# Kernel tuning notes

Measured on AMD Instinct MI355X. Metric: run time of the kernel, lower is better.

Reference implementation:

```python
import jax, jax.numpy as jnp
import numpy as np

N = 262144
E = N * 32
C_W = 7.0 / np.pi  # Wendland C2 2D normalization


def kernel_gradient(q, dirs, h):
    # torchSPHv2 wendland gradient: -dir * C/h^3 * 20 q (1-q)^3, q = r/h in [0,1]
    mag = (C_W / h ** 3) * 20.0 * q * (1.0 - q) ** 3
    return -dirs * mag[:, None]


def setup_inputs() -> dict:
    key = jax.random.key(0)
    ks = jax.random.split(key, 10)
    pos = lambda k: jax.random.uniform(k, (N,), dtype=jnp.float32) + 0.5  # keep strictly positive
    fluidArea = pos(ks[0]) * 1e-3
    fluidActualArea = pos(ks[1]) * 1e-3
    fluidRestDensity = pos(ks[2]) * 1000.0
    fluidDensity = pos(ks[3])
    fluidPressure2 = jax.random.uniform(ks[4], (N,), dtype=jnp.float32) * 1e3
    fluidPredictedVelocity = jax.random.normal(ks[5], (N, 2), dtype=jnp.float32)
    fluidPredAccel = jax.random.normal(ks[6], (N, 2), dtype=jnp.float32)
    fluidNeighbors = jax.random.randint(ks[7], (2, E), 0, N, dtype=jnp.int32)
    fluidRadialDistances = jax.random.uniform(ks[8], (E,), dtype=jnp.float32)
    d = jax.random.normal(ks[9], (E, 2), dtype=jnp.float32)
    fluidDistances = d / (jnp.linalg.norm(d, axis=1, keepdims=True) + 1e-7)
    return {
        'fluidArea': fluidArea, 'fluidActualArea': fluidActualArea,
        'fluidRestDensity': fluidRestDensity, 'fluidDensity': fluidDensity,
        'fluidPressure2': fluidPressure2,
        'fluidPredictedVelocity': fluidPredictedVelocity,
        'fluidPredAccel': fluidPredAccel,
        'fluidRadialDistances': fluidRadialDistances,
        'fluidDistances': fluidDistances,
        'fluidNeighbors': fluidNeighbors,
        'support': 0.05, 'dt': 0.002,
    }


def reference(fluidArea, fluidActualArea, fluidRestDensity, fluidDensity,
              fluidPressure2, fluidPredictedVelocity, fluidPredAccel,
              fluidRadialDistances, fluidDistances, fluidNeighbors,
              support, dt):
    seg = lambda v, i: jax.ops.segment_sum(v, i, num_segments=N)
    i = fluidNeighbors[0]
    j = fluidNeighbors[1]
    grad = kernel_gradient(fluidRadialDistances, fluidDistances, support)  # [E,2]
    grad2 = jnp.einsum('nd,nd->n', grad, grad)

    # --- alpha (fluid term + final) ---
    kSum1 = seg(fluidActualArea[j][:, None] * grad, i)                       # [N,2]
    kSum2 = seg((fluidActualArea ** 2 / (fluidArea * fluidRestDensity))[j] * grad2, i)
    fac = -dt ** 2 * fluidActualArea
    mass = fluidArea * fluidRestDensity
    alpha = fac / mass * jnp.einsum('nd,nd->n', kSum1, kSum1) + fac * kSum2

    # --- fluid pressure acceleration ---
    facA = -(fluidArea * fluidRestDensity)[j]
    p = fluidPressure2 / (fluidDensity * fluidRestDensity) ** 2
    fluidAccelTerm = seg((facA * (p[i] + p[j]))[:, None] * grad, i)          # [N,2]

    # --- source term (velocity divergence) ---
    facS = -dt * fluidActualArea[j]
    vij = fluidPredictedVelocity[i] - fluidPredictedVelocity[j]
    source = seg(facS * jnp.einsum('nd,nd->n', vij, grad), i)                # [N]

    # --- updated pressure fluid kernel sum ---
    facP = dt ** 2 * fluidActualArea[j]
    aij = fluidPredAccel[i] - fluidPredAccel[j]
    kernelSum = seg(jnp.einsum('nd,nd->n', facP[:, None] * aij, grad), i)    # [N]

    return jnp.concatenate([alpha[:, None], fluidAccelTerm,
                            source[:, None], kernelSum[:, None]], axis=1)  # [N,5]
```

## Files before the change

### kernel.cpp

```cpp
#include <hip/hip_runtime.h>
#include <math.h>


#define PB        512
#define PB_SHIFT  9
#define SLICES    8
#define CSTRIDE   16
#define BIN_EPT   8
#define BIN_EDGES (256 * BIN_EPT)
#define TILE      512

typedef float v2f __attribute__((ext_vector_type(2)));

__device__ __forceinline__ void gload_lds16(const float4* g, float4* l) {
    __builtin_amdgcn_global_load_lds(
        (const __attribute__((address_space(1))) void*)g,
        (__attribute__((address_space(3))) void*)l, 16, 0, 0);
}

static inline size_t align256(size_t x) { return (x + 255) & ~(size_t)255; }

__global__ __launch_bounds__(256) void pre_kernel(
    const float*  __restrict__ area,
    const float*  __restrict__ actualArea,
    const float*  __restrict__ restDensity,
    const float*  __restrict__ density,
    const float*  __restrict__ pressure2,
    const float2* __restrict__ vel,
    const float2* __restrict__ accel,
    float4* __restrict__ pre2,
    int*    __restrict__ cursor, int ncursor,
    float*  __restrict__ accz, int nacc,
    int n) {
    int t = blockIdx.x * blockDim.x + threadIdx.x;
    if (t < ncursor) cursor[t] = 0;
    for (int k = t; k < nacc; k += gridDim.x * blockDim.x) accz[k] = 0.f;
    if (t >= n) return;
    float m  = area[t] * restDensity[t];
    float dr = density[t] * restDensity[t];
    float p  = pressure2[t] / (dr * dr);
    float aa = actualArea[t];
    float2 v  = vel[t];
    float2 ac = accel[t];
    pre2[2 * (size_t)t]     = make_float4(p, m / aa, aa, aa * aa / m);
    pre2[2 * (size_t)t + 1] = make_float4(v.x, v.y, ac.x, ac.y);
}

__global__ __launch_bounds__(256) void bin_kernel(
    const int*    __restrict__ nbr,
    const float*  __restrict__ rad,
    const float2* __restrict__ dirs,
    const float*  __restrict__ supp,
    int*          __restrict__ cursor,
    float4*       __restrict__ pay,
    int cap, int nb, int estart, int eend, int E) {
    __shared__ float4 srec[BIN_EDGES];
    __shared__ int lcount[512];
    __shared__ int lclaim[512];
    __shared__ int lstart[512];
    int tid = threadIdx.x;
    for (int k = tid; k < 512; k += 256) lcount[k] = 0;
    __syncthreads();
    int e0 = estart + blockIdx.x * BIN_EDGES + tid;

    int jj[BIN_EPT]; float qq[BIN_EPT]; v2f dd[BIN_EPT]; int pack[BIN_EPT];
#pragma unroll
    for (int k = 0; k < BIN_EPT; ++k) {
        int e = e0 + k * 256;
        pack[k] = -1; jj[k] = 0; qq[k] = 0.f; dd[k] = (v2f){0.f, 0.f};
        if (e < eend) {
            jj[k] = __builtin_nontemporal_load(nbr + E + e);
            qq[k] = __builtin_nontemporal_load(rad + e);
            dd[k] = __builtin_nontemporal_load((const v2f*)dirs + e);
            int i = __builtin_nontemporal_load(nbr + e);
            int b = i >> PB_SHIFT;
            int r = atomicAdd(&lcount[b], 1);
            pack[k] = (b << 22) | ((i & (PB - 1)) << 12) | r;
        }
    }
    __syncthreads();
    for (int k = tid; k < nb; k += 256) {
        int c = lcount[k];
        lclaim[k] = c ? atomicAdd(&cursor[(size_t)k * CSTRIDE], c) : 0;
    }
    if (tid < 64) {
        int running = 0;
        for (int c = 0; c < 8; ++c) {
            int orig = lcount[c * 64 + tid];
            int v = orig;
#pragma unroll
            for (int off = 1; off < 64; off <<= 1) {
                int u = __shfl_up(v, off, 64);
                if (tid >= off) v += u;
            }
            lstart[c * 64 + tid] = running + v - orig;
            running += __shfl(v, 63, 64);
        }
    }
    __syncthreads();

    float h  = supp[0];
    float kc = 20.0f * (7.0f / 3.14159265358979323846f) / (h * h * h);

#pragma unroll
    for (int k = 0; k < BIN_EPT; ++k) {
        if (pack[k] < 0) continue;
        int b  = pack[k] >> 22;
        int li = (pack[k] >> 12) & (PB - 1);
        int r  = pack[k] & 4095;
        float  q = qq[k];
        v2f    d = dd[k];
        float om  = 1.0f - q;
        float mag = kc * q * om * om * om;
        float gx = -d.x * mag;
        float gy = -d.y * mag;
        int jli  = (jj[k] << 9) | li;
        int cb   = lclaim[b];
        int gi   = (cb + r < cap) ? (b * cap + cb + r) : -1;
        srec[lstart[b] + r] = make_float4(__int_as_float(jli), gx, gy,
                                          __int_as_float(gi));
    }
    __syncthreads();
    int total = lstart[511] + lcount[511];
    for (int t = tid; t < total; t += 256) {
        float4 rec = srec[t];
        int gi = __float_as_int(rec.w);
        if (gi >= 0) pay[gi] = make_float4(rec.x, rec.y, rec.z, 0.f);
    }
}

__global__ __launch_bounds__(256) void reduce_kernel(
    const float4* __restrict__ pay,
    const int*    __restrict__ cursor, int cap,
    const float4* __restrict__ pre2,
    const float*  __restrict__ dtp,
    float*        __restrict__ partials,
    int spc, int soff, int n) {
    __shared__ float4 stage[TILE];
    __shared__ float4 sorted[TILE * 2];
    __shared__ int    lhist[PB];
    __shared__ int    lofs[PB];
    int b   = blockIdx.x / spc;
    int s   = blockIdx.x % spc;
    int tid = threadIdx.x;

    int p0 = (b << PB_SHIFT) + tid;
    int p1 = p0 + 256;
    float pi0 = (p0 < n) ? pre2[2 * (size_t)p0].x : 0.f;
    float pi1 = (p1 < n) ? pre2[2 * (size_t)p1].x : 0.f;
    float a0[7] = {0.f, 0.f, 0.f, 0.f, 0.f, 0.f, 0.f};
    float a1[7] = {0.f, 0.f, 0.f, 0.f, 0.f, 0.f, 0.f};
    float dt  = dtp[0];
    float dt2 = dt * dt;

    int cnt = cursor[(size_t)b * CSTRIDE];
    if (cnt > cap) cnt = cap;
    int lo = (int)((long long)cnt * s / spc);
    int hi = (int)((long long)cnt * (s + 1) / spc);
    size_t base = (size_t)b * cap;

    for (int T = lo; T < hi; T += TILE) {
#pragma unroll
        for (int si = 0; si < 2; ++si) {
            int fl  = (si << 8) + tid;
            int rec = T + fl;
            size_t g = (rec < hi) ? (base + rec) : base;
            gload_lds16(pay + g, stage + fl);
        }
        __syncthreads();
        lhist[tid] = 0; lhist[tid + 256] = 0;
        float4 r0 = stage[tid];
        float4 r1 = stage[tid + 256];
        bool v0 = (T + tid) < hi;
        bool v1 = (T + tid + 256) < hi;
        int jli0 = __float_as_int(r0.x);
        int jli1 = __float_as_int(r1.x);
        int li0 = jli0 & (PB - 1);
        int li1 = jli1 & (PB - 1);
        size_t j0 = (size_t)(v0 ? (jli0 >> 9) : 0);
        size_t j1 = (size_t)(v1 ? (jli1 >> 9) : 0);
        float4 ja0 = pre2[2 * j0], jb0 = pre2[2 * j0 + 1];
        float4 ja1 = pre2[2 * j1], jb1 = pre2[2 * j1 + 1];
        __syncthreads();
        if (v0) atomicAdd(&lhist[li0], 1);
        if (v1) atomicAdd(&lhist[li1], 1);
        __syncthreads();
        if (tid < 64) {
            int running = 0;
            for (int c = 0; c < 8; ++c) {
                int orig = lhist[c * 64 + tid];
                int v = orig;
#pragma unroll
                for (int off = 1; off < 64; off <<= 1) {
                    int u = __shfl_up(v, off, 64);
                    if (tid >= off) v += u;
                }
                lofs[c * 64 + tid] = running + v - orig;
                running += __shfl(v, 63, 64);
            }
        }
        __syncthreads();
        if (v0) {
            int slot = atomicAdd(&lofs[li0], 1);
            float c0 = ja0.z * r0.y;
            float c1 = ja0.z * r0.z;
            float c2 = ja0.w * (r0.y * r0.y + r0.z * r0.z);
            float q5 = dt  * (jb0.x * c0 + jb0.y * c1);
            float q6 = dt2 * (jb0.z * c0 + jb0.w * c1);
            sorted[2 * slot]     = make_float4(c0, c1, c2, ja0.y);
            sorted[2 * slot + 1] = make_float4(ja0.x, q5, q6, 0.f);
        }
        if (v1) {
            int slot = atomicAdd(&lofs[li1], 1);
            float c0 = ja1.z * r1.y;
            float c1 = ja1.z * r1.z;
            float c2 = ja1.w * (r1.y * r1.y + r1.z * r1.z);
            float q5 = dt  * (jb1.x * c0 + jb1.y * c1);
            float q6 = dt2 * (jb1.z * c0 + jb1.w * c1);
            sorted[2 * slot]     = make_float4(c0, c1, c2, ja1.y);
            sorted[2 * slot + 1] = make_float4(ja1.x, q5, q6, 0.f);
        }
        __syncthreads();
        {
            int end0 = lofs[tid];
            for (int r = end0 - lhist[tid]; r < end0; ++r) {
                float4 e0 = sorted[2 * r];
                float4 e1 = sorted[2 * r + 1];
                float rc = -(pi0 + e1.x) * e0.w;
                a0[0] += e0.x; a0[1] += e0.y; a0[2] += e0.z;
                a0[3] += rc * e0.x; a0[4] += rc * e0.y;
                a0[5] += e1.y; a0[6] += e1.z;
            }
            int end1 = lofs[tid + 256];
            for (int r = end1 - lhist[tid + 256]; r < end1; ++r) {
                float4 e0 = sorted[2 * r];
                float4 e1 = sorted[2 * r + 1];
                float rc = -(pi1 + e1.x) * e0.w;
                a1[0] += e0.x; a1[1] += e0.y; a1[2] += e0.z;
                a1[3] += rc * e0.x; a1[4] += rc * e0.y;
                a1[5] += e1.y; a1[6] += e1.z;
            }
        }
    }

    float* dst = partials + ((size_t)b * SLICES + soff + s) * (PB * 7);
    {
        float4 va = (p0 < n) ? pre2[2 * (size_t)p0 + 1]
                             : make_float4(0.f, 0.f, 0.f, 0.f);
        float src = a0[5] - dt  * (va.x * a0[0] + va.y * a0[1]);
        float ker = dt2 * (va.z * a0[0] + va.w * a0[1]) - a0[6];
        float* d = dst + (size_t)tid * 7;
        d[0] = a0[0]; d[1] = a0[1]; d[2] = a0[2]; d[3] = a0[3]; d[4] = a0[4];
        d[5] = src;   d[6] = ker;
    }
    {
        float4 va = (p1 < n) ? pre2[2 * (size_t)p1 + 1]
                             : make_float4(0.f, 0.f, 0.f, 0.f);
        float src = a1[5] - dt  * (va.x * a1[0] + va.y * a1[1]);
        float ker = dt2 * (va.z * a1[0] + va.w * a1[1]) - a1[6];
        float* d = dst + (size_t)(tid + 256) * 7;
        d[0] = a1[0]; d[1] = a1[1]; d[2] = a1[2]; d[3] = a1[3]; d[4] = a1[4];
        d[5] = src;   d[6] = ker;
    }
}

__global__ void edge_kernel(const int* __restrict__ nbr,
                            const float* __restrict__ rad,
                            const float2* __restrict__ dirs,
                            const float4* __restrict__ pre2,
                            const float* __restrict__ supp,
                            const float* __restrict__ dtp,
                            float* __restrict__ acc, int E) {
    int e = blockIdx.x * blockDim.x + threadIdx.x;
    if (e >= E) return;
    float h = supp[0], dt = dtp[0];
    float kc = 20.0f * (7.0f / 3.14159265358979323846f) / (h * h * h);
    int i = nbr[e];
    int j = nbr[E + e];
    float  q = rad[e];
    float2 d = dirs[e];
    float om  = 1.0f - q;
    float mag = kc * q * om * om * om;
    float gx = -d.x * mag;
    float gy = -d.y * mag;
    float g2 = gx * gx + gy * gy;
    float4 ja = pre2[2 * (size_t)j];
    float4 jb = pre2[2 * (size_t)j + 1];
    float4 ia = pre2[2 * (size_t)i];
    float4 ib = pre2[2 * (size_t)i + 1];
    float aaj = ja.z;
    float m   = ja.y * aaj;
    float pp  = -m * (ia.x + ja.x);
    float vdotg = (ib.x - jb.x) * gx + (ib.y - jb.y) * gy;
    float adotg = (ib.z - jb.z) * gx + (ib.w - jb.w) * gy;
    float* base = acc + (size_t)i * 8;
    atomicAdd(base + 0, aaj * gx);
    atomicAdd(base + 1, aaj * gy);
    atomicAdd(base + 2, ja.w * g2);
    atomicAdd(base + 3, pp * gx);
    atomicAdd(base + 4, pp * gy);
    atomicAdd(base + 5, -dt * aaj * vdotg);
    atomicAdd(base + 6, dt * dt * aaj * adotg);
}

__global__ __launch_bounds__(256) void fin_kernel(
    const float* __restrict__ area,
    const float* __restrict__ actualArea,
    const float* __restrict__ restDensity,
    const float* __restrict__ dtp,
    const float* __restrict__ data, int mode,
    float* __restrict__ out, int n) {
    int t = blockIdx.x * blockDim.x + threadIdx.x;
    if (t >= n) return;
    float s0 = 0, s1 = 0, s2 = 0, s3 = 0, s4 = 0, s5 = 0, s6 = 0;
    if (mode == 0) {
        const float* base = data + ((size_t)(t >> PB_SHIFT) * SLICES) * (PB * 7)
                                 + (size_t)(t & (PB - 1)) * 7;
#pragma unroll
        for (int s = 0; s < SLICES; ++s) {
            const float* p = base + (size_t)s * (PB * 7);
            s0 += p[0]; s1 += p[1]; s2 += p[2]; s3 += p[3];
            s4 += p[4]; s5 += p[5]; s6 += p[6];
        }
    } else {
        const float* a = data + (size_t)t * 8;
        s0 = a[0]; s1 = a[1]; s2 = a[2]; s3 = a[3];
        s4 = a[4]; s5 = a[5]; s6 = a[6];
    }
    float dt   = dtp[0];
    float fac  = -dt * dt * actualArea[t];
    float mass = area[t] * restDensity[t];
    float alpha = fac / mass * (s0 * s0 + s1 * s1) + fac * s2;
    float* o = out + (size_t)t * 5;
    o[0] = alpha;
    o[1] = s3;
    o[2] = s4;
    o[3] = s5;
    o[4] = s6;
}

extern "C" void kernel_launch(void* const* d_in, const int* in_sizes, int n_in,
                              void* d_out, int out_size, void* d_ws, size_t ws_size,
                              hipStream_t stream) {
    const float* area        = (const float*)d_in[0];
    const float* actualArea  = (const float*)d_in[1];
    const float* restDensity = (const float*)d_in[2];
    const float* density     = (const float*)d_in[3];
    const float* pressure2   = (const float*)d_in[4];
    const float2* vel        = (const float2*)d_in[5];
    const float2* accel      = (const float2*)d_in[6];
    const float* rad         = (const float*)d_in[7];
    const float2* dirs       = (const float2*)d_in[8];
    const int*   nbr         = (const int*)d_in[9];
    const float* supp        = (const float*)d_in[10];
    const float* dtp         = (const float*)d_in[11];
    float* out = (float*)d_out;

    int N = in_sizes[0];
    int E = in_sizes[7];
    int nb = (N + PB - 1) >> PB_SHIFT;

    size_t sz_cur   = (size_t)nb * CSTRIDE * 8 * sizeof(int);
    size_t off_pre  = align256(sz_cur);
    size_t sz_pre   = (size_t)N * 8 * sizeof(float);
    size_t off_part = align256(off_pre + sz_pre);
    size_t sz_part  = (size_t)nb * SLICES * PB * 7 * sizeof(float);
    size_t off_pay  = align256(off_part + sz_part);

    int* cursor     = (int*)d_ws;
    float4* pre2    = (float4*)((char*)d_ws + off_pre);
    float* partials = (float*)((char*)d_ws + off_part);

    int nchunk = 0, cap = 0;
    if (nb <= 512 && ws_size > off_pay) {
        for (int c = 1; c <= 8; c *= 2) {
            long long Ec = (E + c - 1) / c;
            double mean = (double)Ec / (double)nb;
            long long need = (long long)(mean + 8.0 * sqrt(mean) + 128.0);
            need = (need + 63) & ~63ll;
            if (off_pay + (size_t)nb * need * 16 <= ws_size) {
                nchunk = c; cap = (int)need; break;
            }
        }
    }

    int bs = 256;
    int grid_n = (N + bs - 1) / bs;
    if (nchunk > 0) {
        float4* pay = (float4*)((char*)d_ws + off_pay);
        int ncursor = nb * CSTRIDE * nchunk;
        pre_kernel<<<grid_n, bs, 0, stream>>>(
            area, actualArea, restDensity, density, pressure2, vel, accel,
            pre2, cursor, ncursor, (float*)nullptr, 0, N);
        int spc = SLICES / nchunk; if (spc < 1) spc = 1;
        int Ec  = (E + nchunk - 1) / nchunk;
        for (int c = 0; c < nchunk; ++c) {
            int es = c * Ec;
            int ee = es + Ec; if (ee > E) ee = E;
            if (es >= ee) break;
            int* curC = cursor + (size_t)c * nb * CSTRIDE;
            int nblk = (ee - es + BIN_EDGES - 1) / BIN_EDGES;
            bin_kernel<<<nblk, bs, 0, stream>>>(
                nbr, rad, dirs, supp, curC, pay, cap, nb, es, ee, E);
            reduce_kernel<<<nb * spc, bs, 0, stream>>>(
                pay, curC, cap, pre2, dtp, partials, spc, c * spc, N);
        }
        fin_kernel<<<grid_n, bs, 0, stream>>>(
            area, actualArea, restDensity, dtp, partials, 0, out, N);
    } else {
        float* acc = partials;
        pre_kernel<<<grid_n, bs, 0, stream>>>(
            area, actualArea, restDensity, density, pressure2, vel, accel,
            pre2, cursor, 0, acc, N * 8, N);
        edge_kernel<<<(E + bs - 1) / bs, bs, 0, stream>>>(
            nbr, rad, dirs, pre2, supp, dtp, acc, E);
        fin_kernel<<<grid_n, bs, 0, stream>>>(
            area, actualArea, restDensity, dtp, acc, 1, out, N);
    }
}
```

Before: 418.4 us.

## Double-buffer reduce tile loads and process bin edges in two halves

The reduce kernel now prefetches the next payload tile into a second LDS buffer while the current tile is processed, and uses a custom barrier that waits only on LDS counters. The bin kernel handles twice as many edges per block in two halves with separate counters, so the LDS record buffer stays the same size while fewer blocks make global cursor atomics. Slices per bucket drop from 8 to 4, which halves reduce blocks and the partials read in fin. The risks are lower parallelism in reduce, higher register pressure in bin, and the custom barrier skipping the vmcnt wait on the prefetched global-to-LDS loads.

```diff
diff --git a/kernel.cpp b/kernel.cpp
--- a/kernel.cpp
+++ b/kernel.cpp
@@ -6,7 +6,7 @@
 #define PB_SHIFT  9
 #define SLICES    8
 #define CSTRIDE   16
-#define BIN_EPT   8
+#define BIN_EPT   16
 #define BIN_EDGES (256 * BIN_EPT)
 #define TILE      512
 
@@ -16,6 +16,12 @@
     __builtin_amdgcn_global_load_lds(
         (const __attribute__((address_space(1))) void*)g,
         (__attribute__((address_space(3))) void*)l, 16, 0, 0);
+}
+
+__device__ __forceinline__ void ldsbar() {
+    asm volatile("s_waitcnt lgkmcnt(0)" ::: "memory");
+    __builtin_amdgcn_s_barrier();
+    asm volatile("" ::: "memory");
 }
 
 static inline size_t align256(size_t x) { return (x + 255) & ~(size_t)255; }
@@ -54,60 +60,66 @@
     int*          __restrict__ cursor,
     float4*       __restrict__ pay,
     int cap, int nb, int estart, int eend, int E) {
-    __shared__ float4 srec[BIN_EDGES];
-    __shared__ int lcount[512];
+    __shared__ float4 srec[2048];
+    __shared__ int lcntA[512];
+    __shared__ int lcntB[512];
     __shared__ int lclaim[512];
-    __shared__ int lstart[512];
+    __shared__ int lstartA[512];
+    __shared__ int lstartB[512];
     int tid = threadIdx.x;
-    for (int k = tid; k < 512; k += 256) lcount[k] = 0;
-    __syncthreads();
-    int e0 = estart + blockIdx.x * BIN_EDGES + tid;
-
-    int jj[BIN_EPT]; float qq[BIN_EPT]; v2f dd[BIN_EPT]; int pack[BIN_EPT];
+    for (int k = tid; k < 512; k += 256) { lcntA[k] = 0; lcntB[k] = 0; }
+    ldsbar();
+    int eb = estart + blockIdx.x * BIN_EDGES + tid;
+
+    int jj[BIN_EPT]; float qq[BIN_EPT]; v2f dd[BIN_EPT]; int pk[BIN_EPT];
 #pragma unroll
     for (int k = 0; k < BIN_EPT; ++k) {
-        int e = e0 + k * 256;
-        pack[k] = -1; jj[k] = 0; qq[k] = 0.f; dd[k] = (v2f){0.f, 0.f};
+        int e = eb + k * 256;
+        pk[k] = -1; jj[k] = 0; qq[k] = 0.f; dd[k] = (v2f){0.f, 0.f};
         if (e < eend) {
             jj[k] = __builtin_nontemporal_load(nbr + E + e);
             qq[k] = __builtin_nontemporal_load(rad + e);
             dd[k] = __builtin_nontemporal_load((const v2f*)dirs + e);
             int i = __builtin_nontemporal_load(nbr + e);
             int b = i >> PB_SHIFT;
-            int r = atomicAdd(&lcount[b], 1);
-            pack[k] = (b << 22) | ((i & (PB - 1)) << 12) | r;
-        }
-    }
-    __syncthreads();
-    for (int k = tid; k < nb; k += 256) {
-        int c = lcount[k];
-        lclaim[k] = c ? atomicAdd(&cursor[(size_t)k * CSTRIDE], c) : 0;
-    }
-    if (tid < 64) {
-        int running = 0;
+            int r = (k < 8) ? atomicAdd(&lcntA[b], 1) : atomicAdd(&lcntB[b], 1);
+            pk[k] = (b << 22) | ((i & (PB - 1)) << 12) | r;
+        }
+    }
+    ldsbar();
+    if (tid >= 64) {
+        for (int k = tid - 64; k < nb; k += 192) {
+            int c = lcntA[k] + lcntB[k];
+            lclaim[k] = c ? atomicAdd(&cursor[(size_t)k * CSTRIDE], c) : 0;
+        }
+    } else {
+        int runA = 0, runB = 0;
         for (int c = 0; c < 8; ++c) {
-            int orig = lcount[c * 64 + tid];
-            int v = orig;
+            int oA = lcntA[c * 64 + tid]; int vA = oA;
+            int oB = lcntB[c * 64 + tid]; int vB = oB;
 #pragma unroll
             for (int off = 1; off < 64; off <<= 1) {
-                int u = __shfl_up(v, off, 64);
-                if (tid >= off) v += u;
-            }
-            lstart[c * 64 + tid] = running + v - orig;
-            running += __shfl(v, 63, 64);
-        }
-    }
-    __syncthreads();
+                int uA = __shfl_up(vA, off, 64);
+                int uB = __shfl_up(vB, off, 64);
+                if (tid >= off) { vA += uA; vB += uB; }
+            }
+            lstartA[c * 64 + tid] = runA + vA - oA;
+            lstartB[c * 64 + tid] = runB + vB - oB;
+            runA += __shfl(vA, 63, 64);
+            runB += __shfl(vB, 63, 64);
+        }
+    }
+    ldsbar();
 
     float h  = supp[0];
     float kc = 20.0f * (7.0f / 3.14159265358979323846f) / (h * h * h);
 
 #pragma unroll
-    for (int k = 0; k < BIN_EPT; ++k) {
-        if (pack[k] < 0) continue;
-        int b  = pack[k] >> 22;
-        int li = (pack[k] >> 12) & (PB - 1);
-        int r  = pack[k] & 4095;
+    for (int k = 0; k < 8; ++k) {
+        if (pk[k] < 0) continue;
+        int b  = pk[k] >> 22;
+        int li = (pk[k] >> 12) & (PB - 1);
+        int r  = pk[k] & 4095;
         float  q = qq[k];
         v2f    d = dd[k];
         float om  = 1.0f - q;
@@ -115,17 +127,47 @@
         float gx = -d.x * mag;
         float gy = -d.y * mag;
         int jli  = (jj[k] << 9) | li;
-        int cb   = lclaim[b];
-        int gi   = (cb + r < cap) ? (b * cap + cb + r) : -1;
-        srec[lstart[b] + r] = make_float4(__int_as_float(jli), gx, gy,
-                                          __int_as_float(gi));
-    }
-    __syncthreads();
-    int total = lstart[511] + lcount[511];
-    for (int t = tid; t < total; t += 256) {
-        float4 rec = srec[t];
-        int gi = __float_as_int(rec.w);
-        if (gi >= 0) pay[gi] = make_float4(rec.x, rec.y, rec.z, 0.f);
+        int g    = lclaim[b] + r;
+        int gi   = (g < cap) ? (b * cap + g) : -1;
+        srec[lstartA[b] + r] = make_float4(__int_as_float(jli), gx, gy,
+                                           __int_as_float(gi));
+    }
+    ldsbar();
+    {
+        int total = lstartA[511] + lcntA[511];
+        for (int t = tid; t < total; t += 256) {
+            float4 rec = srec[t];
+            int gi = __float_as_int(rec.w);
+            if (gi >= 0) pay[gi] = make_float4(rec.x, rec.y, rec.z, 0.f);
+        }
+    }
+    ldsbar();
+#pragma unroll
+    for (int k = 8; k < BIN_EPT; ++k) {
+        if (pk[k] < 0) continue;
+        int b  = pk[k] >> 22;
+        int li = (pk[k] >> 12) & (PB - 1);
+        int r  = pk[k] & 4095;
+        float  q = qq[k];
+        v2f    d = dd[k];
+        float om  = 1.0f - q;
+        float mag = kc * q * om * om * om;
+        float gx = -d.x * mag;
+        float gy = -d.y * mag;
+        int jli  = (jj[k] << 9) | li;
+        int g    = lclaim[b] + lcntA[b] + r;
+        int gi   = (g < cap) ? (b * cap + g) : -1;
+        srec[lstartB[b] + r] = make_float4(__int_as_float(jli), gx, gy,
+                                           __int_as_float(gi));
+    }
+    ldsbar();
+    {
+        int total = lstartB[511] + lcntB[511];
+        for (int t = tid; t < total; t += 256) {
+            float4 rec = srec[t];
+            int gi = __float_as_int(rec.w);
+            if (gi >= 0) pay[gi] = make_float4(rec.x, rec.y, rec.z, 0.f);
+        }
     }
 }
 
@@ -136,7 +178,7 @@
     const float*  __restrict__ dtp,
     float*        __restrict__ partials,
     int spc, int soff, int n) {
-    __shared__ float4 stage[TILE];
+    __shared__ float4 stage[2][TILE];
     __shared__ float4 sorted[TILE * 2];
     __shared__ int    lhist[PB];
     __shared__ int    lofs[PB];
@@ -159,18 +201,21 @@
     int hi = (int)((long long)cnt * (s + 1) / spc);
     size_t base = (size_t)b * cap;
 
-    for (int T = lo; T < hi; T += TILE) {
+    if (lo < hi) {
 #pragma unroll
         for (int si = 0; si < 2; ++si) {
             int fl  = (si << 8) + tid;
-            int rec = T + fl;
+            int rec = lo + fl;
             size_t g = (rec < hi) ? (base + rec) : base;
-            gload_lds16(pay + g, stage + fl);
-        }
+            gload_lds16(pay + g, &stage[0][fl]);
+        }
+    }
+    int cur = 0;
+    for (int T = lo; T < hi; T += TILE) {
         __syncthreads();
         lhist[tid] = 0; lhist[tid + 256] = 0;
-        float4 r0 = stage[tid];
-        float4 r1 = stage[tid + 256];
+        float4 r0 = stage[cur][tid];
+        float4 r1 = stage[cur][tid + 256];
         bool v0 = (T + tid) < hi;
         bool v1 = (T + tid + 256) < hi;
         int jli0 = __float_as_int(r0.x);
@@ -181,10 +226,20 @@
         size_t j1 = (size_t)(v1 ? (jli1 >> 9) : 0);
         float4 ja0 = pre2[2 * j0], jb0 = pre2[2 * j0 + 1];
         float4 ja1 = pre2[2 * j1], jb1 = pre2[2 * j1 + 1];
-        __syncthreads();
+        int Tn = T + TILE;
+        if (Tn < hi) {
+#pragma unroll
+            for (int si = 0; si < 2; ++si) {
+                int fl  = (si << 8) + tid;
+                int rec = Tn + fl;
+                size_t g = (rec < hi) ? (base + rec) : base;
+                gload_lds16(pay + g, &stage[cur ^ 1][fl]);
+            }
+        }
+        ldsbar();
         if (v0) atomicAdd(&lhist[li0], 1);
         if (v1) atomicAdd(&lhist[li1], 1);
-        __syncthreads();
+        ldsbar();
         if (tid < 64) {
             int running = 0;
             for (int c = 0; c < 8; ++c) {
@@ -199,7 +254,7 @@
                 running += __shfl(v, 63, 64);
             }
         }
-        __syncthreads();
+        ldsbar();
         if (v0) {
             int slot = atomicAdd(&lofs[li0], 1);
             float c0 = ja0.z * r0.y;
@@ -220,7 +275,7 @@
             sorted[2 * slot]     = make_float4(c0, c1, c2, ja1.y);
             sorted[2 * slot + 1] = make_float4(ja1.x, q5, q6, 0.f);
         }
-        __syncthreads();
+        ldsbar();
         {
             int end0 = lofs[tid];
             for (int r = end0 - lhist[tid]; r < end0; ++r) {
@@ -241,6 +296,7 @@
                 a1[5] += e1.y; a1[6] += e1.z;
             }
         }
+        cur ^= 1;
     }
 
     float* dst = partials + ((size_t)b * SLICES + soff + s) * (PB * 7);
@@ -308,7 +364,7 @@
     const float* __restrict__ actualArea,
     const float* __restrict__ restDensity,
     const float* __restrict__ dtp,
-    const float* __restrict__ data, int mode,
+    const float* __restrict__ data, int mode, int nslice,
     float* __restrict__ out, int n) {
     int t = blockIdx.x * blockDim.x + threadIdx.x;
     if (t >= n) return;
@@ -316,8 +372,7 @@
     if (mode == 0) {
         const float* base = data + ((size_t)(t >> PB_SHIFT) * SLICES) * (PB * 7)
                                  + (size_t)(t & (PB - 1)) * 7;
-#pragma unroll
-        for (int s = 0; s < SLICES; ++s) {
+        for (int s = 0; s < nslice; ++s) {
             const float* p = base + (size_t)s * (PB * 7);
             s0 += p[0]; s1 += p[1]; s2 += p[2]; s3 += p[3];
             s4 += p[4]; s5 += p[5]; s6 += p[6];
@@ -392,7 +447,8 @@
         pre_kernel<<<grid_n, bs, 0, stream>>>(
             area, actualArea, restDensity, density, pressure2, vel, accel,
             pre2, cursor, ncursor, (float*)nullptr, 0, N);
-        int spc = SLICES / nchunk; if (spc < 1) spc = 1;
+        int spc = 4 / nchunk; if (spc < 1) spc = 1;
+        int nslice = spc * nchunk;
         int Ec  = (E + nchunk - 1) / nchunk;
         for (int c = 0; c < nchunk; ++c) {
             int es = c * Ec;
@@ -406,7 +462,7 @@
                 pay, curC, cap, pre2, dtp, partials, spc, c * spc, N);
         }
         fin_kernel<<<grid_n, bs, 0, stream>>>(
-            area, actualArea, restDensity, dtp, partials, 0, out, N);
+            area, actualArea, restDensity, dtp, partials, 0, nslice, out, N);
     } else {
         float* acc = partials;
         pre_kernel<<<grid_n, bs, 0, stream>>>(
@@ -415,6 +471,6 @@
         edge_kernel<<<(E + bs - 1) / bs, bs, 0, stream>>>(
             nbr, rad, dirs, pre2, supp, dtp, acc, E);
         fin_kernel<<<grid_n, bs, 0, stream>>>(
-            area, actualArea, restDensity, dtp, acc, 1, out, N);
-    }
-}
+            area, actualArea, restDensity, dtp, acc, 1,0, out, N);
+    }
+}
```

Result: slower. 481.3 us (+15.0%).

## Shard bins into per-block sub-buckets with 12-byte payload and wider reduce tiles

Applied to the files above, without the earlier changes.

Bin_kernel now writes into 8 sub-buckets per particle block, keyed by the bin block index, so cursor atomics contend less. The payload record shrinks from 16 to 12 bytes and is written as dword scatters. Reduce_kernel processes one sub-bucket per block with 1024-record tiles, loads the next tile from registers ahead of use, and stores sorted contributions as a structure-of-arrays with the pressure factor precomputed. It also replaces __syncthreads with custom lgkmcnt barriers and accumulates across chunks. The risks are 3-way uncoalesced stores, possible overflow of the smaller per-sub-bucket capacity, and a larger LDS footprint that may lower occupancy.

```diff
diff --git a/kernel.cpp b/kernel.cpp
--- a/kernel.cpp
+++ b/kernel.cpp
@@ -6,16 +6,16 @@
 #define PB_SHIFT  9
 #define SLICES    8
 #define CSTRIDE   16
-#define BIN_EPT   8
-#define BIN_EDGES (256 * BIN_EPT)
-#define TILE      512
+#define NR        8
+#define BIN_EDGES 2048
+#define TILE      1024
 
 typedef float v2f __attribute__((ext_vector_type(2)));
 
-__device__ __forceinline__ void gload_lds16(const float4* g, float4* l) {
-    __builtin_amdgcn_global_load_lds(
-        (const __attribute__((address_space(1))) void*)g,
-        (__attribute__((address_space(3))) void*)l, 16, 0, 0);
+__device__ __forceinline__ void ldsbar() {
+    asm volatile("s_waitcnt lgkmcnt(0)" ::: "memory");
+    __builtin_amdgcn_s_barrier();
+    asm volatile("" ::: "memory");
 }
 
 static inline size_t align256(size_t x) { return (x + 255) & ~(size_t)255; }
@@ -33,8 +33,9 @@
     float*  __restrict__ accz, int nacc,
     int n) {
     int t = blockIdx.x * blockDim.x + threadIdx.x;
-    if (t < ncursor) cursor[t] = 0;
-    for (int k = t; k < nacc; k += gridDim.x * blockDim.x) accz[k] = 0.f;
+    int stride = gridDim.x * blockDim.x;
+    for (int k = t; k < ncursor; k += stride) cursor[k] = 0;
+    for (int k = t; k < nacc; k += stride) accz[k] = 0.f;
     if (t >= n) return;
     float m  = area[t] * restDensity[t];
     float dr = density[t] * restDensity[t];
@@ -52,22 +53,24 @@
     const float2* __restrict__ dirs,
     const float*  __restrict__ supp,
     int*          __restrict__ cursor,
-    float4*       __restrict__ pay,
+    unsigned int* __restrict__ pay32,
     int cap, int nb, int estart, int eend, int E) {
-    __shared__ float4 srec[BIN_EDGES];
+    __shared__ float s3[BIN_EDGES * 3];
+    __shared__ int   sD[BIN_EDGES];
     __shared__ int lcount[512];
     __shared__ int lclaim[512];
     __shared__ int lstart[512];
     int tid = threadIdx.x;
+    int x   = blockIdx.x & (NR - 1);
     for (int k = tid; k < 512; k += 256) lcount[k] = 0;
-    __syncthreads();
+    ldsbar();
     int e0 = estart + blockIdx.x * BIN_EDGES + tid;
 
-    int jj[BIN_EPT]; float qq[BIN_EPT]; v2f dd[BIN_EPT]; int pack[BIN_EPT];
+    int jj[8]; float qq[8]; v2f dd[8]; int pk[8];
 #pragma unroll
-    for (int k = 0; k < BIN_EPT; ++k) {
+    for (int k = 0; k < 8; ++k) {
         int e = e0 + k * 256;
-        pack[k] = -1; jj[k] = 0; qq[k] = 0.f; dd[k] = (v2f){0.f, 0.f};
+        pk[k] = -1; jj[k] = 0; qq[k] = 0.f; dd[k] = (v2f){0.f, 0.f};
         if (e < eend) {
             jj[k] = __builtin_nontemporal_load(nbr + E + e);
             qq[k] = __builtin_nontemporal_load(rad + e);
@@ -75,15 +78,16 @@
             int i = __builtin_nontemporal_load(nbr + e);
             int b = i >> PB_SHIFT;
             int r = atomicAdd(&lcount[b], 1);
-            pack[k] = (b << 22) | ((i & (PB - 1)) << 12) | r;
-        }
-    }
-    __syncthreads();
-    for (int k = tid; k < nb; k += 256) {
-        int c = lcount[k];
-        lclaim[k] = c ? atomicAdd(&cursor[(size_t)k * CSTRIDE], c) : 0;
-    }
-    if (tid < 64) {
+            pk[k] = (b << 21) | ((i & (PB - 1)) << 12) | r;
+        }
+    }
+    ldsbar();
+    if (tid >= 64) {
+        for (int k = tid - 64; k < nb; k += 192) {
+            int c = lcount[k];
+            lclaim[k] = c ? atomicAdd(&cursor[(size_t)(k * NR + x) * CSTRIDE], c) : 0;
+        }
+    } else {
         int running = 0;
         for (int c = 0; c < 8; ++c) {
             int orig = lcount[c * 64 + tid];
@@ -97,94 +101,109 @@
             running += __shfl(v, 63, 64);
         }
     }
-    __syncthreads();
+    ldsbar();
 
     float h  = supp[0];
     float kc = 20.0f * (7.0f / 3.14159265358979323846f) / (h * h * h);
+    int cap3  = cap * 3;
+    int cap24 = cap * 3 * NR;
 
 #pragma unroll
-    for (int k = 0; k < BIN_EPT; ++k) {
-        if (pack[k] < 0) continue;
-        int b  = pack[k] >> 22;
-        int li = (pack[k] >> 12) & (PB - 1);
-        int r  = pack[k] & 4095;
+    for (int k = 0; k < 8; ++k) {
+        if (pk[k] < 0) continue;
+        int b  = pk[k] >> 21;
+        int li = (pk[k] >> 12) & (PB - 1);
+        int r  = pk[k] & 2047;
         float  q = qq[k];
         v2f    d = dd[k];
         float om  = 1.0f - q;
         float mag = kc * q * om * om * om;
         float gx = -d.x * mag;
         float gy = -d.y * mag;
-        int jli  = (jj[k] << 9) | li;
-        int cb   = lclaim[b];
-        int gi   = (cb + r < cap) ? (b * cap + cb + r) : -1;
-        srec[lstart[b] + r] = make_float4(__int_as_float(jli), gx, gy,
-                                          __int_as_float(gi));
-    }
-    __syncthreads();
-    int total = lstart[511] + lcount[511];
-    for (int t = tid; t < total; t += 256) {
-        float4 rec = srec[t];
-        int gi = __float_as_int(rec.w);
-        if (gi >= 0) pay[gi] = make_float4(rec.x, rec.y, rec.z, 0.f);
+        int slot = lstart[b] + r;
+        s3[slot * 3 + 0] = __int_as_float((jj[k] << PB_SHIFT) | li);
+        s3[slot * 3 + 1] = gx;
+        s3[slot * 3 + 2] = gy;
+        int g = lclaim[b] + r;
+        sD[slot] = (g < cap) ? (b * cap24 + x * cap3 + g * 3) : -1;
+    }
+    ldsbar();
+    int total3 = (lstart[511] + lcount[511]) * 3;
+    for (int dwi = tid; dwi < total3; dwi += 256) {
+        int rec = dwi / 3;
+        int f   = dwi - rec * 3;
+        int gd  = sD[rec];
+        if (gd >= 0) pay32[gd + f] = __float_as_uint(s3[dwi]);
     }
 }
 
 __global__ __launch_bounds__(256) void reduce_kernel(
-    const float4* __restrict__ pay,
+    const unsigned int* __restrict__ pay32,
     const int*    __restrict__ cursor, int cap,
     const float4* __restrict__ pre2,
     const float*  __restrict__ dtp,
     float*        __restrict__ partials,
-    int spc, int soff, int n) {
-    __shared__ float4 stage[TILE];
-    __shared__ float4 sorted[TILE * 2];
-    __shared__ int    lhist[PB];
-    __shared__ int    lofs[PB];
-    int b   = blockIdx.x / spc;
-    int s   = blockIdx.x % spc;
+    int accum, int n) {
+    __shared__ float s7[7][TILE];
+    __shared__ int   lhist[PB];
+    __shared__ int   lofs[PB];
+    __shared__ float ptab[PB];
+    int b   = blockIdx.x >> 3;
+    int s   = blockIdx.x & (NR - 1);
     int tid = threadIdx.x;
 
     int p0 = (b << PB_SHIFT) + tid;
     int p1 = p0 + 256;
     float pi0 = (p0 < n) ? pre2[2 * (size_t)p0].x : 0.f;
     float pi1 = (p1 < n) ? pre2[2 * (size_t)p1].x : 0.f;
+    ptab[tid] = pi0; ptab[tid + 256] = pi1;
     float a0[7] = {0.f, 0.f, 0.f, 0.f, 0.f, 0.f, 0.f};
     float a1[7] = {0.f, 0.f, 0.f, 0.f, 0.f, 0.f, 0.f};
     float dt  = dtp[0];
     float dt2 = dt * dt;
 
-    int cnt = cursor[(size_t)b * CSTRIDE];
+    int cnt = cursor[(size_t)(b * NR + s) * CSTRIDE];
     if (cnt > cap) cnt = cap;
-    int lo = (int)((long long)cnt * s / spc);
-    int hi = (int)((long long)cnt * (s + 1) / spc);
-    size_t base = (size_t)b * cap;
-
-    for (int T = lo; T < hi; T += TILE) {
-#pragma unroll
-        for (int si = 0; si < 2; ++si) {
-            int fl  = (si << 8) + tid;
-            int rec = T + fl;
-            size_t g = (rec < hi) ? (base + rec) : base;
-            gload_lds16(pay + g, stage + fl);
-        }
-        __syncthreads();
+    size_t RB = (size_t)(b * NR + s) * cap * 3;
+    int r0 = tid * 4;
+
+    float4 c0v, c1v, c2v, n0v, n1v, n2v;
+    if (cnt > 0) {
+        int rb = r0;
+        int rc_ = (rb + 4 <= cap) ? rb : (cap - 4);
+        const float4* g = (const float4*)(pay32 + RB + (size_t)rc_ * 3);
+        c0v = g[0]; c1v = g[1]; c2v = g[2];
+    }
+    for (int T = 0; T < cnt; T += TILE) {
         lhist[tid] = 0; lhist[tid + 256] = 0;
-        float4 r0 = stage[tid];
-        float4 r1 = stage[tid + 256];
-        bool v0 = (T + tid) < hi;
-        bool v1 = (T + tid + 256) < hi;
-        int jli0 = __float_as_int(r0.x);
-        int jli1 = __float_as_int(r1.x);
-        int li0 = jli0 & (PB - 1);
-        int li1 = jli1 & (PB - 1);
-        size_t j0 = (size_t)(v0 ? (jli0 >> 9) : 0);
-        size_t j1 = (size_t)(v1 ? (jli1 >> 9) : 0);
+        if (T + TILE < cnt) {
+            int rb = T + TILE + r0;
+            int rc_ = (rb + 4 <= cap) ? rb : (cap - 4);
+            const float4* g = (const float4*)(pay32 + RB + (size_t)rc_ * 3);
+            n0v = g[0]; n1v = g[1]; n2v = g[2];
+        }
+        int rb = T + r0;
+        bool v0 = rb < cnt, v1 = rb + 1 < cnt, v2 = rb + 2 < cnt, v3 = rb + 3 < cnt;
+        int jli0 = __float_as_int(c0v.x); float gx0 = c0v.y, gy0 = c0v.z;
+        int jli1 = __float_as_int(c0v.w); float gx1 = c1v.x, gy1 = c1v.y;
+        int jli2 = __float_as_int(c1v.z); float gx2 = c1v.w, gy2 = c2v.x;
+        int jli3 = __float_as_int(c2v.y); float gx3 = c2v.z, gy3 = c2v.w;
+        int li0 = jli0 & (PB - 1), li1 = jli1 & (PB - 1);
+        int li2 = jli2 & (PB - 1), li3 = jli3 & (PB - 1);
+        size_t j0 = v0 ? (size_t)(jli0 >> PB_SHIFT) : 0;
+        size_t j1 = v1 ? (size_t)(jli1 >> PB_SHIFT) : 0;
+        size_t j2 = v2 ? (size_t)(jli2 >> PB_SHIFT) : 0;
+        size_t j3 = v3 ? (size_t)(jli3 >> PB_SHIFT) : 0;
         float4 ja0 = pre2[2 * j0], jb0 = pre2[2 * j0 + 1];
         float4 ja1 = pre2[2 * j1], jb1 = pre2[2 * j1 + 1];
-        __syncthreads();
+        float4 ja2 = pre2[2 * j2], jb2 = pre2[2 * j2 + 1];
+        float4 ja3 = pre2[2 * j3], jb3 = pre2[2 * j3 + 1];
+        ldsbar();
         if (v0) atomicAdd(&lhist[li0], 1);
         if (v1) atomicAdd(&lhist[li1], 1);
-        __syncthreads();
+        if (v2) atomicAdd(&lhist[li2], 1);
+        if (v3) atomicAdd(&lhist[li3], 1);
+        ldsbar();
         if (tid < 64) {
             int running = 0;
             for (int c = 0; c < 8; ++c) {
@@ -199,59 +218,57 @@
                 running += __shfl(v, 63, 64);
             }
         }
-        __syncthreads();
-        if (v0) {
-            int slot = atomicAdd(&lofs[li0], 1);
-            float c0 = ja0.z * r0.y;
-            float c1 = ja0.z * r0.z;
-            float c2 = ja0.w * (r0.y * r0.y + r0.z * r0.z);
-            float q5 = dt  * (jb0.x * c0 + jb0.y * c1);
-            float q6 = dt2 * (jb0.z * c0 + jb0.w * c1);
-            sorted[2 * slot]     = make_float4(c0, c1, c2, ja0.y);
-            sorted[2 * slot + 1] = make_float4(ja0.x, q5, q6, 0.f);
-        }
-        if (v1) {
-            int slot = atomicAdd(&lofs[li1], 1);
-            float c0 = ja1.z * r1.y;
-            float c1 = ja1.z * r1.z;
-            float c2 = ja1.w * (r1.y * r1.y + r1.z * r1.z);
-            float q5 = dt  * (jb1.x * c0 + jb1.y * c1);
-            float q6 = dt2 * (jb1.z * c0 + jb1.w * c1);
-            sorted[2 * slot]     = make_float4(c0, c1, c2, ja1.y);
-            sorted[2 * slot + 1] = make_float4(ja1.x, q5, q6, 0.f);
-        }
-        __syncthreads();
+        ldsbar();
+#define SCAT(vv, li, jaa, jbb, gxx, gyy)                                     \
+        if (vv) {                                                            \
+            int sl = atomicAdd(&lofs[li], 1);                                \
+            float C0 = jaa.z * gxx;                                          \
+            float C1 = jaa.z * gyy;                                          \
+            float C2 = jaa.w * (gxx * gxx + gyy * gyy);                      \
+            float rc = -(ptab[li] + jaa.x) * jaa.y;                          \
+            s7[0][sl] = C0;      s7[1][sl] = C1;      s7[2][sl] = C2;        \
+            s7[3][sl] = rc * C0; s7[4][sl] = rc * C1;                        \
+            s7[5][sl] = dt  * (jbb.x * C0 + jbb.y * C1);                     \
+            s7[6][sl] = dt2 * (jbb.z * C0 + jbb.w * C1);                     \
+        }
+        SCAT(v0, li0, ja0, jb0, gx0, gy0)
+        SCAT(v1, li1, ja1, jb1, gx1, gy1)
+        SCAT(v2, li2, ja2, jb2, gx2, gy2)
+        SCAT(v3, li3, ja3, jb3, gx3, gy3)
+#undef SCAT
+        ldsbar();
         {
-            int end0 = lofs[tid];
-            for (int r = end0 - lhist[tid]; r < end0; ++r) {
-                float4 e0 = sorted[2 * r];
-                float4 e1 = sorted[2 * r + 1];
-                float rc = -(pi0 + e1.x) * e0.w;
-                a0[0] += e0.x; a0[1] += e0.y; a0[2] += e0.z;
-                a0[3] += rc * e0.x; a0[4] += rc * e0.y;
-                a0[5] += e1.y; a0[6] += e1.z;
+            int e0 = lofs[tid], h0 = lhist[tid];
+            for (int r = e0 - h0; r < e0; ++r) {
+                a0[0] += s7[0][r]; a0[1] += s7[1][r]; a0[2] += s7[2][r];
+                a0[3] += s7[3][r]; a0[4] += s7[4][r];
+                a0[5] += s7[5][r]; a0[6] += s7[6][r];
             }
-            int end1 = lofs[tid + 256];
-            for (int r = end1 - lhist[tid + 256]; r < end1; ++r) {
-                float4 e0 = sorted[2 * r];
-                float4 e1 = sorted[2 * r + 1];
-                float rc = -(pi1 + e1.x) * e0.w;
-                a1[0] += e0.x; a1[1] += e0.y; a1[2] += e0.z;
-                a1[3] += rc * e0.x; a1[4] += rc * e0.y;
-                a1[5] += e1.y; a1[6] += e1.z;
+            int e1 = lofs[tid + 256], h1 = lhist[tid + 256];
+            for (int r = e1 - h1; r < e1; ++r) {
+                a1[0] += s7[0][r]; a1[1] += s7[1][r]; a1[2] += s7[2][r];
+                a1[3] += s7[3][r]; a1[4] += s7[4][r];
+                a1[5] += s7[5][r]; a1[6] += s7[6][r];
             }
         }
-    }
-
-    float* dst = partials + ((size_t)b * SLICES + soff + s) * (PB * 7);
+        ldsbar();
+        c0v = n0v; c1v = n1v; c2v = n2v;
+    }
+
+    float* dst = partials + ((size_t)b * SLICES + s) * (PB * 7);
     {
         float4 va = (p0 < n) ? pre2[2 * (size_t)p0 + 1]
                              : make_float4(0.f, 0.f, 0.f, 0.f);
         float src = a0[5] - dt  * (va.x * a0[0] + va.y * a0[1]);
         float ker = dt2 * (va.z * a0[0] + va.w * a0[1]) - a0[6];
         float* d = dst + (size_t)tid * 7;
-        d[0] = a0[0]; d[1] = a0[1]; d[2] = a0[2]; d[3] = a0[3]; d[4] = a0[4];
-        d[5] = src;   d[6] = ker;
+        if (accum) {
+            d[0] += a0[0]; d[1] += a0[1]; d[2] += a0[2]; d[3] += a0[3];
+            d[4] += a0[4]; d[5] += src;   d[6] += ker;
+        } else {
+            d[0] = a0[0]; d[1] = a0[1]; d[2] = a0[2]; d[3] = a0[3];
+            d[4] = a0[4]; d[5] = src;   d[6] = ker;
+        }
     }
     {
         float4 va = (p1 < n) ? pre2[2 * (size_t)p1 + 1]
@@ -259,8 +276,13 @@
         float src = a1[5] - dt  * (va.x * a1[0] + va.y * a1[1]);
         float ker = dt2 * (va.z * a1[0] + va.w * a1[1]) - a1[6];
         float* d = dst + (size_t)(tid + 256) * 7;
-        d[0] = a1[0]; d[1] = a1[1]; d[2] = a1[2]; d[3] = a1[3]; d[4] = a1[4];
-        d[5] = src;   d[6] = ker;
+        if (accum) {
+            d[0] += a1[0]; d[1] += a1[1]; d[2] += a1[2]; d[3] += a1[3];
+            d[4] += a1[4]; d[5] += src;   d[6] += ker;
+        } else {
+            d[0] = a1[0]; d[1] = a1[1]; d[2] = a1[2]; d[3] = a1[3];
+            d[4] = a1[4]; d[5] = src;   d[6] = ker;
+        }
     }
 }
 
@@ -308,7 +330,7 @@
     const float* __restrict__ actualArea,
     const float* __restrict__ restDensity,
     const float* __restrict__ dtp,
-    const float* __restrict__ data, int mode,
+    const float* __restrict__ data, int mode, int nslice,
     float* __restrict__ out, int n) {
     int t = blockIdx.x * blockDim.x + threadIdx.x;
     if (t >= n) return;
@@ -316,8 +338,7 @@
     if (mode == 0) {
         const float* base = data + ((size_t)(t >> PB_SHIFT) * SLICES) * (PB * 7)
                                  + (size_t)(t & (PB - 1)) * 7;
-#pragma unroll
-        for (int s = 0; s < SLICES; ++s) {
+        for (int s = 0; s < nslice; ++s) {
             const float* p = base + (size_t)s * (PB * 7);
             s0 += p[0]; s1 += p[1]; s2 += p[2]; s3 += p[3];
             s4 += p[4]; s5 += p[5]; s6 += p[6];
@@ -360,7 +381,7 @@
     int E = in_sizes[7];
     int nb = (N + PB - 1) >> PB_SHIFT;
 
-    size_t sz_cur   = (size_t)nb * CSTRIDE * 8 * sizeof(int);
+    size_t sz_cur   = (size_t)nb * NR * CSTRIDE * 8 * sizeof(int);
     size_t off_pre  = align256(sz_cur);
     size_t sz_pre   = (size_t)N * 8 * sizeof(float);
     size_t off_part = align256(off_pre + sz_pre);
@@ -375,10 +396,10 @@
     if (nb <= 512 && ws_size > off_pay) {
         for (int c = 1; c <= 8; c *= 2) {
             long long Ec = (E + c - 1) / c;
-            double mean = (double)Ec / (double)nb;
-            long long need = (long long)(mean + 8.0 * sqrt(mean) + 128.0);
+            double mean = (double)Ec / ((double)nb * NR);
+            long long need = (long long)(mean + 8.0 * sqrt(mean) + 64.0);
             need = (need + 63) & ~63ll;
-            if (off_pay + (size_t)nb * need * 16 <= ws_size) {
+            if (off_pay + (size_t)nb * NR * need * 12 <= ws_size) {
                 nchunk = c; cap = (int)need; break;
             }
         }
@@ -387,26 +408,25 @@
     int bs = 256;
     int grid_n = (N + bs - 1) / bs;
     if (nchunk > 0) {
-        float4* pay = (float4*)((char*)d_ws + off_pay);
-        int ncursor = nb * CSTRIDE * nchunk;
+        unsigned int* pay32 = (unsigned int*)((char*)d_ws + off_pay);
+        int ncursor = nb * NR * CSTRIDE * nchunk;
         pre_kernel<<<grid_n, bs, 0, stream>>>(
             area, actualArea, restDensity, density, pressure2, vel, accel,
             pre2, cursor, ncursor, (float*)nullptr, 0, N);
-        int spc = SLICES / nchunk; if (spc < 1) spc = 1;
         int Ec  = (E + nchunk - 1) / nchunk;
         for (int c = 0; c < nchunk; ++c) {
             int es = c * Ec;
             int ee = es + Ec; if (ee > E) ee = E;
             if (es >= ee) break;
-            int* curC = cursor + (size_t)c * nb * CSTRIDE;
+            int* curC = cursor + (size_t)c * nb * NR * CSTRIDE;
             int nblk = (ee - es + BIN_EDGES - 1) / BIN_EDGES;
             bin_kernel<<<nblk, bs, 0, stream>>>(
-                nbr, rad, dirs, supp, curC, pay, cap, nb, es, ee, E);
-            reduce_kernel<<<nb * spc, bs, 0, stream>>>(
-                pay, curC, cap, pre2, dtp, partials, spc, c * spc, N);
+                nbr, rad, dirs, supp, curC, pay32, cap, nb, es, ee, E);
+            reduce_kernel<<<nb * NR, bs, 0, stream>>>(
+                pay32, curC, cap, pre2, dtp, partials, (c > 0) ? 1 : 0, N);
         }
         fin_kernel<<<grid_n, bs, 0, stream>>>(
-            area, actualArea, restDensity, dtp, partials, 0, out, N);
+            area, actualArea, restDensity, dtp, partials, 0, SLICES, out, N);
     } else {
         float* acc = partials;
         pre_kernel<<<grid_n, bs, 0, stream>>>(
@@ -415,6 +435,6 @@
         edge_kernel<<<(E + bs - 1) / bs, bs, 0, stream>>>(
             nbr, rad, dirs, pre2, supp, dtp, acc, E);
         fin_kernel<<<grid_n, bs, 0, stream>>>(
-            area, actualArea, restDensity, dtp, acc, 1, out, N);
-    }
-}
+            area, actualArea, restDensity, dtp, acc, 1, 0, out, N);
+    }
+}
```

New measurement: 397.9 us. 4.9% less time.
